# Kernel optimization log

Hardware: AMD Instinct MI355X
Metric: run time of the kernel (lower is better)

## Reference

```python
import jax, jax.numpy as jnp
import numpy as np

V = 131072          # total vertices (hits) across all events
K = 64              # neighbours per vertex, col 0 == self
NSEG = 4            # number of events (row splits segments)
THRESHOLD = 0.5     # hierarchy score cut (layer's non-trainable threshold var)


def setup_inputs() -> dict:
    key = jax.random.key(0)
    k1, k2 = jax.random.split(key)
    score = jax.random.uniform(k1, (V, 1), dtype=jnp.float32)
    seg = V // NSEG
    base = (jnp.arange(V, dtype=jnp.int32) // seg) * seg
    # random neighbours constrained to the same segment; column 0 is self
    rnd = jax.random.randint(k2, (V, K - 1), 0, seg, dtype=jnp.int32) + base[:, None]
    nidxs = jnp.concatenate([jnp.arange(V, dtype=jnp.int32)[:, None], rnd], axis=1)
    row_splits = (jnp.arange(NSEG + 1, dtype=jnp.int32) * seg)
    return {"score": score, "nidxs": nidxs, "row_splits": row_splits}


def _local_group(score1, nidxs, row_splits, thr):
    """Greedy threshold-based neighbour grouping (HGCalML LocalGroup op).

    Vertices are visited per segment in descending score order. An unused
    vertex becomes a group seed; if its score > thr it absorbs all of its
    not-yet-used neighbours. Returns fixed-shape (-1 padded) outputs so the
    whole thing is jit-compatible.
    """
    V_, K_ = nidxs.shape
    seg_id = jnp.searchsorted(row_splits, jnp.arange(V_, dtype=row_splits.dtype),
                              side='right') - 1
    # per-segment descending-score order == tf.argsort(DESC) per row split
    order = jnp.lexsort((-score1, seg_id)).astype(jnp.int32)
    kcols = jnp.arange(K_)

    def step(state, v):
        used, assign, dirn, sel, seed, count = state
        is_new = jnp.logical_not(used[v])                 # v not grouped yet -> seed
        expand = score1[v] > thr                          # absorb neighbours?
        cand = jnp.where(expand, nidxs[v],
                         jnp.where(kcols == 0, v, -1))    # else only self
        safe = jnp.clip(cand, 0, V_ - 1)
        valid = (cand >= 0) & jnp.logical_not(used[safe]) & is_new
        used = used.at[safe].set(used[safe] | valid)
        assign = assign.at[safe].set(jnp.where(valid, count, assign[safe]))
        dirn = dirn.at[v].set(jnp.where(valid, cand, -1))
        sel = sel.at[count].set(jnp.where(is_new, v, sel[count]))
        seed = seed.at[v].set(seed[v] | is_new)
        count = count + is_new.astype(jnp.int32)
        return (used, assign, dirn, sel, seed, count), None

    init = (jnp.zeros(V_, dtype=bool),                 # used
            jnp.full(V_, -1, jnp.int32),               # backgather: seed rank per vertex
            jnp.full((V_, K_), -1, jnp.int32),         # directed neighbour idxs
            jnp.full(V_, -1, jnp.int32),               # selected seed vertices, -1 padded
            jnp.zeros(V_, dtype=bool),                 # seed mask
            jnp.int32(0))
    (used, assign, dirn, sel, seed, count), _ = jax.lax.scan(step, init, order)
    cs0 = jnp.concatenate([jnp.zeros(1, jnp.int32),
                           jnp.cumsum(seed.astype(jnp.int32))])
    rs_new = cs0[row_splits]                           # new row splits over seeds
    return rs_new, dirn, sel[:, None], assign, count


def reference(score, nidxs, row_splits):
    # layer: score = clip(score, 0, 1); per-segment argsort; LocalGroup
    score1 = jnp.clip(score.reshape(-1), 0.0, 1.0)
    rs_new, dirnidx, sel, backgather, n_sel = _local_group(score1, nidxs,
                                                           row_splits, THRESHOLD)
    # return_backscatter=True -> back = [V, sel]; we return sel (padded) + n_sel
    # outputs: directed nidx (V,K), selection idxs (V,1 padded with -1),
    #          backgather (V,), new row splits, number selected
    return dirnidx, sel, backgather, rs_new, n_sel
```

## Files before the change

kernel.cpp:

```cpp
#include <hip/hip_runtime.h>
#include <stdint.h>

#define INFU 0xFFFFFFFFu
#define LCAP 32768
#define POSCAP 20480
#define NC 128

__global__ void __launch_bounds__(256) k_hist(const float* score, unsigned* bcnt,
                                              unsigned* claim, int* sel, unsigned* segE,
                                              int V, int SEGN, int initClaim){
  int v = blockIdx.x*blockDim.x+threadIdx.x; if (v>=V) return;
  if (initClaim) claim[v]=INFU;
  sel[v]=-1;
  float s = score[v]; s = fminf(fmaxf(s,0.f),1.f);
  int seg = v / SEGN;
  bool ex = (s > 0.5f);
  unsigned long long act = __ballot(true);
  unsigned long long mex = __ballot(ex);
  int lane = threadIdx.x & 63;
  int seg0 = __shfl(seg, 0);
  bool uni = (act == ~0ull) && (__shfl(seg,63) == seg0);
  if (uni){
    if (lane==0 && mex) atomicAdd(&segE[seg0], (unsigned)__popcll(mex));
  } else {
    if (ex) atomicAdd(&segE[seg], 1u);
  }
  int b = (int)(s*(float)SEGN); if (b>=SEGN) b=SEGN-1; if (b<0) b=0;
  int bd = SEGN-1-b;
  atomicAdd(&bcnt[(size_t)seg*SEGN+bd], 1u);
}

__global__ void __launch_bounds__(1024) k_scan0(const unsigned* bcnt, unsigned* bbase,
                                                unsigned* bfill, int SEGN){
  int seg = blockIdx.x; int tid = threadIdx.x; int lane = tid&63, wv = tid>>6;
  __shared__ unsigned s_wc[1024];
  const size_t base = (size_t)seg*SEGN;
  const int NP = (SEGN+1023)>>10;
  for (int p=0;p<NP;p++){
    int i = p*1024 + tid;
    unsigned x = (i<SEGN)? bcnt[base+i] : 0u;
    unsigned incl = x;
    #pragma unroll
    for (int off=1;off<64;off<<=1){ unsigned t=__shfl_up(incl,(unsigned)off); if (lane>=off) incl+=t; }
    if (lane==63) s_wc[p*16+wv]=incl;
  }
  __syncthreads();
  if (wv==0){
    unsigned carry=0; int n=NP*16;
    for (int ch=0; ch*64<n; ch++){
      int idx=ch*64+lane;
      unsigned x=(idx<n)? s_wc[idx]:0u;
      unsigned incl=x;
      #pragma unroll
      for (int off=1;off<64;off<<=1){ unsigned t=__shfl_up(incl,(unsigned)off); if (lane>=off) incl+=t; }
      if (idx<n) s_wc[idx]=carry+incl-x;
      carry += __shfl(incl,63);
    }
  }
  __syncthreads();
  for (int p=0;p<NP;p++){
    int i = p*1024 + tid;
    if (i<SEGN){
      unsigned x = bcnt[base+i];
      unsigned incl = x;
      #pragma unroll
      for (int off=1;off<64;off<<=1){ unsigned t=__shfl_up(incl,(unsigned)off); if (lane>=off) incl+=t; }
      bbase[base+i] = s_wc[p*16+wv] + incl - x;
      bfill[base+i] = 0u;
    }
  }
}

__global__ void __launch_bounds__(1024) k_scan(const unsigned* in, const unsigned* claim,
                                               unsigned* outExcl, unsigned* segTotal,
                                               int SEGN, int mode){
  int seg = blockIdx.x; int tid = threadIdx.x; int lane = tid&63, wv = tid>>6;
  __shared__ unsigned wsum[16];
  const int CH = (SEGN+1023)>>10;
  int i0 = tid*CH, i1 = i0+CH; if (i1>SEGN) i1=SEGN;
  const size_t base = (size_t)seg*SEGN;
  unsigned sum=0;
  for (int i=i0;i<i1;i++){
    unsigned x = (mode==0)? in[base+i] : ((claim[base+i]==INFU)?1u:0u);
    sum+=x;
  }
  unsigned incl=sum;
  for (int off=1;off<64;off<<=1){ unsigned t=__shfl_up(incl,(unsigned)off); if (lane>=off) incl+=t; }
  if (lane==63) wsum[wv]=incl;
  __syncthreads();
  unsigned wbase=0,total=0;
  for (int w=0;w<16;w++){ unsigned s=wsum[w]; if (w<wv) wbase+=s; total+=s; }
  unsigned run = wbase + incl - sum;
  for (int i=i0;i<i1;i++){
    unsigned x = (mode==0)? in[base+i] : ((claim[base+i]==INFU)?1u:0u);
    outExcl[base+i]=run; run+=x;
  }
  if (tid==0 && segTotal) segTotal[seg]=total;
}

__global__ void __launch_bounds__(256) k_scatter(const float* score, const unsigned* bbase,
                                                 unsigned* bfill, unsigned long long* slot,
                                                 int V, int SEGN){
  int v = blockIdx.x*blockDim.x+threadIdx.x; if (v>=V) return;
  float s = score[v]; s=fminf(fmaxf(s,0.f),1.f);
  int b=(int)(s*(float)SEGN); if(b>=SEGN)b=SEGN-1; if(b<0)b=0;
  int bd=SEGN-1-b; int seg=v/SEGN;
  size_t bk = (size_t)seg*SEGN+bd;
  unsigned pos = bbase[bk] + atomicAdd(&bfill[bk],1u);
  unsigned kb = ~__float_as_uint(s);
  slot[(size_t)seg*SEGN+pos] = ((unsigned long long)kb<<32) | (unsigned)v;
}

__global__ void __launch_bounds__(256) k_bsortbuild(const unsigned* bcnt, const unsigned* bbase,
                                                    unsigned long long* slot,
                                                    int* ord, unsigned* rnkv,
                                                    int V, int SEGN){
  int t = blockIdx.x*blockDim.x+threadIdx.x; if (t>=V) return;
  unsigned n = bcnt[t];
  if (!n) return;
  int seg = t / SEGN;
  const size_t segbase = (size_t)seg*SEGN;
  unsigned base = bbase[t];
  unsigned long long* a = slot + segbase + base;
  for (unsigned i=1;i<n;i++){
    unsigned long long key=a[i]; int j=(int)i-1;
    while (j>=0 && a[j]>key){ a[j+1]=a[j]; j--; }
    a[j+1]=key;
  }
  for (unsigned i=0;i<n;i++){
    int v = (int)(unsigned)(a[i] & 0xFFFFFFFFull);
    ord[segbase + base + i] = v;
    rnkv[v] = base + i;
  }
}

__global__ void __launch_bounds__(256) k_pack4(const int* ord, const unsigned* rnkv, const int* nidxs,
                                               const unsigned* segE, unsigned short* nbr16,
                                               int V, int K, int SEGN){
  const int K4 = K>>2;
  long long q = (long long)blockIdx.x*256 + threadIdx.x;
  if (q >= (long long)V*K4) return;
  int gr = (int)(q / K4); int k4 = (int)(q - (long long)gr*K4);
  int seg = gr / SEGN, r = gr - seg*SEGN;
  if (r >= (int)segE[seg]) return;
  int v = ord[gr];
  const int4 nn = *(const int4*)(nidxs + (size_t)v*K + (size_t)k4*4);
  ushort4 o;
  o.x=(unsigned short)rnkv[nn.x]; o.y=(unsigned short)rnkv[nn.y];
  o.z=(unsigned short)rnkv[nn.z]; o.w=(unsigned short)rnkv[nn.w];
  *(ushort4*)(nbr16 + (size_t)gr*K + (size_t)k4*4) = o;
}
__global__ void __launch_bounds__(256) k_pack(const int* ord, const unsigned* rnkv, const int* nidxs,
                                              const unsigned* segE, unsigned short* nbr16,
                                              int V, int K, int SEGN){
  long long t = (long long)blockIdx.x*256 + threadIdx.x;
  if (t >= (long long)V*K) return;
  int gr = (int)(t / K); int k = (int)(t - (long long)gr*K);
  int seg = gr / SEGN, r = gr - seg*SEGN;
  if (r >= (int)segE[seg]) return;
  int v = ord[gr];
  int w = nidxs[(size_t)v*K + k];
  nbr16[t] = (unsigned short)rnkv[w];
}

__global__ void __launch_bounds__(1024) k_greedy(const unsigned short* nbr16, const int* nidxs,
                                                 const int* ord, const unsigned* rnkv,
                                                 const unsigned* segEp,
                                                 unsigned* claim, unsigned* srank,
                                                 unsigned* segTotal, unsigned* absorb,
                                                 int SEGN, int K){
  __shared__ unsigned s_cl[LCAP/2];
  __shared__ unsigned short s_rnk[LCAP];
  __shared__ unsigned char s_pos[POSCAP];
  __shared__ unsigned s_cand[NC];
  __shared__ unsigned long long s_McLo[NC];
  __shared__ unsigned long long s_McHi[NC];
  __shared__ unsigned long long s_anyLo, s_anyHi;
  __shared__ unsigned long long s_bm[16];
  __shared__ unsigned s_ws[16];
  __shared__ unsigned s_base;
  __shared__ unsigned s_wcur;
  __shared__ unsigned long long s_v0, s_v1;
  const int seg = blockIdx.x, tid = threadIdx.x, lane = tid&63, wv = tid>>6;
  unsigned* clg = claim + (size_t)seg*SEGN;
  const size_t segbase = (size_t)seg*SEGN;
  const int E = (int)segEp[seg];
  const int cap = (LCAP < SEGN) ? LCAP : SEGN;
  const bool useDirect = (cap == SEGN);
  const int capw = (cap+1)>>1;
  for (int i=tid; i<capw; i+=1024) s_cl[i]=0xFFFFFFFFu;
  for (int i=tid; i<((POSCAP+3)>>2); i+=1024) ((unsigned*)s_pos)[i]=0u;
  if (useDirect){
    for (int i=tid; i<SEGN; i+=1024) s_rnk[i] = (unsigned short)rnkv[segbase + i];
  }
  if (tid<NC) s_cand[tid]=INFU;
  const unsigned long long lt_mask = (lane==0) ? 0ull : ((~0ull) >> (64-lane));
  const int li = (lane<K)? lane : 0;
  unsigned wcursor = 0;
  for (;;){
    __syncthreads();
    if (tid<NC){
      unsigned pc = s_cand[tid];
      if (pc!=INFU && pc<(unsigned)POSCAP) s_pos[pc]=0;
      s_cand[tid]=INFU; s_McLo[tid]=0ull; s_McHi[tid]=0ull;
    }
    if (tid==NC)   s_anyLo=0ull;
    if (tid==NC+1) s_anyHi=0ull;
    int found = 0;
    for (;;){
      unsigned r = wcursor + (unsigned)(wv*64 + lane);
      bool undec=false;
      if (r<(unsigned)E){
        if (r<(unsigned)cap)
          undec = (((s_cl[r>>1]>>((r&1)*16))&0xFFFFu)==0xFFFFu);
        else
          undec = (__hip_atomic_load(&clg[r], __ATOMIC_RELAXED, __HIP_MEMORY_SCOPE_AGENT)==INFU);
      }
      unsigned long long m = __ballot(undec);
      if (lane==0) s_bm[wv]=m;
      __syncthreads();
      unsigned long long mb = (lane<16)? s_bm[lane] : 0ull;
      int pc16 = (int)__popcll(mb);
      int incl = pc16;
      #pragma unroll
      for (int off=1; off<16; off<<=1){ int t=__shfl_up(incl,off); if (lane>=off) incl+=t; }
      int total = __shfl(incl, 15);
      int below = __shfl(incl, wv) - __shfl(pc16, wv);
      int pos = found + below + (int)__popcll(m & lt_mask);
      if (undec && pos<NC){
        s_cand[pos]=r;
        if (r<(unsigned)POSCAP) s_pos[r]=(unsigned char)(pos+1);
      }
      if (undec && pos==NC-1) s_wcur=r+1;
      bool filled = (found+total>=NC);
      bool winend = (wcursor + 1024 >= (unsigned)E);
      __syncthreads();
      if (filled){ wcursor = s_wcur; found=NC; break; }
      found += total;
      if (winend){ wcursor=(unsigned)E; break; }
      wcursor += 1024;
    }
    const int ncand = found;
    if (!ncand) break;
    unsigned rwq[8], cq[8];
    #pragma unroll
    for (int q=0;q<8;q++){
      int c=(wv<<3)|q;
      cq[q] = (c<ncand) ? s_cand[c] : INFU;
    }
    if (useDirect){
      int vq[8], nq[8];
      #pragma unroll
      for (int q=0;q<8;q++){
        unsigned cc = (cq[q]!=INFU)? cq[q] : 0u;
        vq[q] = ord[segbase + cc];
      }
      #pragma unroll
      for (int q=0;q<8;q++)
        nq[q] = nidxs[(size_t)vq[q]*K + li];
      #pragma unroll
      for (int q=0;q<8;q++){
        unsigned lv = (unsigned)(nq[q] - (int)segbase);
        unsigned rr = s_rnk[lv];
        rwq[q] = (cq[q]!=INFU && lane<K) ? rr : INFU;
      }
    } else {
      #pragma unroll
      for (int q=0;q<8;q++){
        rwq[q]=INFU;
        if (cq[q]!=INFU && lane<K)
          rwq[q] = (unsigned)nbr16[(segbase + cq[q])*K + lane];
      }
    }
    const bool fastmap = (s_cand[ncand-1] < (unsigned)POSCAP);
    #pragma unroll
    for (int q=0;q<8;q++){
      int c=(wv<<3)|q;
      if (cq[q]!=INFU){
        unsigned rw = rwq[q];
        int p = -1;
        if (fastmap){
          if (rw<(unsigned)POSCAP){ p = (int)s_pos[rw] - 1; }
        } else {
          int pp=0;
          if (s_cand[pp+64]<=rw) pp+=64;
          if (s_cand[pp+32]<=rw) pp+=32;
          if (s_cand[pp+16]<=rw) pp+=16;
          if (s_cand[pp+8 ]<=rw) pp+=8;
          if (s_cand[pp+4 ]<=rw) pp+=4;
          if (s_cand[pp+2 ]<=rw) pp+=2;
          if (s_cand[pp+1 ]<=rw) pp+=1;
          if (pp<ncand && s_cand[pp]==rw) p=pp;
        }
        if (lane<K && p>c){
          if (p<64){ atomicOr(&s_McLo[c], 1ull<<p);      atomicOr(&s_anyLo, 1ull<<p); }
          else     { atomicOr(&s_McHi[c], 1ull<<(p-64)); atomicOr(&s_anyHi, 1ull<<(p-64)); }
        }
      }
    }
    __syncthreads();
    if (wv==0){
      const int n0 = (ncand<64)? ncand : 64;
      const int n1 = ncand - n0;
      const unsigned long long nmask0 = (n0==64)? ~0ull : ((1ull<<n0)-1ull);
      unsigned long long Mj0 = s_McLo[lane];
      unsigned long long any0 = s_anyLo & nmask0;
      unsigned long long valid0 = (~any0) & nmask0;
      unsigned long long rem = any0;
      while (rem){
        int i=__builtin_ctzll(rem); rem &= rem-1;
        bool pred = ((valid0>>lane)&1ull) && (lane<i) && ((Mj0>>i)&1ull);
        if (__ballot(pred)==0ull) valid0 |= (1ull<<i);
      }
      unsigned long long valid1 = 0ull;
      if (n1>0){
        const unsigned long long nmask1 = (n1==64)? ~0ull : ((1ull<<n1)-1ull);
        unsigned long long sp = ((valid0>>lane)&1ull) ? s_McHi[lane] : 0ull;
        #pragma unroll
        for (int off=32; off; off>>=1)
          sp |= (unsigned long long)__shfl_xor((long long)sp, off);
        unsigned long long Mj1 = s_McHi[64+lane];
        unsigned long long any1 = s_anyHi & nmask1;
        valid1 = (~(any1|sp)) & nmask1;
        unsigned long long rem1 = any1 & ~sp;
        while (rem1){
          int i=__builtin_ctzll(rem1); rem1 &= rem1-1;
          bool pred = ((valid1>>lane)&1ull) && (lane<i) && ((Mj1>>i)&1ull);
          if (__ballot(pred)==0ull) valid1 |= (1ull<<i);
        }
      }
      if (lane==0){ s_v0=valid0; s_v1=valid1; }
    }
    __syncthreads();
    const unsigned long long v0 = s_v0, v1 = s_v1;
    #pragma unroll
    for (int q=0;q<8;q++){
      int c=(wv<<3)|q;
      bool isv = (c<64) ? (((v0>>c)&1ull)!=0ull) : (((v1>>(c-64))&1ull)!=0ull);
      if (cq[q]!=INFU && isv){
        unsigned rw=rwq[q], cr=cq[q];
        if (rw>cr && rw!=INFU){
          if (rw<(unsigned)cap){
            unsigned idx=rw>>1, sh=(rw&1)*16;
            unsigned old=s_cl[idx];
            for(;;){
              unsigned curv=(old>>sh)&0xFFFFu;
              if (cr>=curv) break;
              unsigned neu=(old & ~(0xFFFFu<<sh)) | (cr<<sh);
              unsigned prev=atomicCAS(&s_cl[idx], old, neu);
              if (prev==old) break;
              old=prev;
            }
          } else {
            atomicMin(&clg[rw], cr);
          }
        }
      }
    }
  }
  __syncthreads();
  if (cap == SEGN){
    if (tid==0) s_base=0;
    __syncthreads();
    for (int p=0; p<cap; p+=1024){
      int i = p + tid;
      bool live = (i<cap);
      unsigned c16 = 0xFFFFu;
      if (live) c16 = (s_cl[i>>1]>>((i&1)*16))&0xFFFFu;
      bool isSeed = live && (c16==0xFFFFu);
      unsigned long long m = __ballot(isSeed);
      if (lane==0) s_ws[wv]=(unsigned)__popcll(m);
      __syncthreads();
      unsigned wbase=0, tot=0;
      for (int w2=0;w2<16;w2++){ unsigned t2=s_ws[w2]; if (w2<wv) wbase+=t2; tot+=t2; }
      unsigned ex = s_base + wbase + (unsigned)__popcll(m & lt_mask);
      if (live){
        srank[segbase + i] = ex;
        absorb[ord[segbase + i]] = isSeed ? (unsigned)i : (unsigned)c16;
      }
      __syncthreads();
      if (tid==0) s_base += tot;
    }
    __syncthreads();
    if (tid==0) segTotal[seg] = s_base;
  } else {
    for (int r=tid; r<cap; r+=1024){
      unsigned c=(s_cl[r>>1]>>((r&1)*16))&0xFFFFu;
      clg[r] = (c==0xFFFFu) ? INFU : c;
    }
  }
}

__global__ void __launch_bounds__(256) k_absorb(const unsigned* rnkv, const unsigned* claim,
                                                unsigned* absorb, int V, int SEGN){
  int v = blockIdx.x*blockDim.x+threadIdx.x; if (v>=V) return;
  int seg = v / SEGN;
  unsigned r = rnkv[v];
  unsigned c = claim[(size_t)seg*SEGN + r];
  absorb[v] = (c==INFU)? r : c;
}

__global__ void __launch_bounds__(256) k_dirnAll4(const int* nidxs, const unsigned* rnkv,
                                                  const unsigned* absorb, const float* score,
                                                  const unsigned* segTotal,
                                                  const unsigned* srank,
                                                  int* dirn, int* sel, int* backg,
                                                  int* rs, int* nsel,
                                                  int V, int K, int SEGN, int NSEG){
  const int K4 = K>>2;
  long long q = (long long)blockIdx.x*256 + threadIdx.x;
  if (q >= (long long)V*K4) return;
  int v = (int)(q / K4); int k4 = (int)(q - (long long)v*K4);
  int seg = v / SEGN;
  if (q <= (long long)NSEG){
    unsigned run=0;
    for (int s=0;s<(int)q;s++) run+=segTotal[s];
    rs[q]=(int)run;
    if ((int)q==NSEG) nsel[0]=(int)run;
  }
  unsigned r = rnkv[v];
  unsigned a_self = absorb[v];
  bool seed = (a_self == r);
  if (k4==0){
    unsigned segOff=0;
    for (int s=0;s<seg;s++) segOff+=segTotal[s];
    unsigned g = segOff + srank[(size_t)seg*SEGN + a_self];
    backg[v] = (int)g;
    if (seed) sel[g] = v;
  }
  int4 o = make_int4(-1,-1,-1,-1);
  if (seed){
    float s = score[v]; s=fminf(fmaxf(s,0.f),1.f);
    if (!(s > 0.5f)){
      if (k4==0) o.x = v;
    } else {
      const int4 nn = *(const int4*)(nidxs + (size_t)v*K + (size_t)k4*4);
      if (absorb[nn.x]==r) o.x=nn.x;
      if (absorb[nn.y]==r) o.y=nn.y;
      if (absorb[nn.z]==r) o.z=nn.z;
      if (absorb[nn.w]==r) o.w=nn.w;
    }
  }
  *(int4*)(dirn + (size_t)v*K + (size_t)k4*4) = o;
}
__global__ void __launch_bounds__(256) k_dirnAll(const int* nidxs, const unsigned* rnkv,
                                                 const unsigned* absorb, const float* score,
                                                 const unsigned* segTotal,
                                                 const unsigned* srank,
                                                 int* dirn, int* sel, int* backg,
                                                 int* rs, int* nsel,
                                                 int V, int K, int SEGN, int NSEG){
  long long t = (long long)blockIdx.x*blockDim.x + threadIdx.x;
  if (t >= (long long)V*K) return;
  int v = (int)(t / K); int j = (int)(t - (long long)v*K);
  int seg = v / SEGN;
  if (t <= (long long)NSEG){
    unsigned run=0;
    for (int s=0;s<(int)t;s++) run+=segTotal[s];
    rs[t]=(int)run;
    if ((int)t==NSEG) nsel[0]=(int)run;
  }
  unsigned r = rnkv[v];
  unsigned a_self = absorb[v];
  bool seed = (a_self == r);
  if (j==0){
    unsigned segOff=0;
    for (int s=0;s<seg;s++) segOff+=segTotal[s];
    unsigned g = segOff + srank[(size_t)seg*SEGN + a_self];
    backg[v] = (int)g;
    if (seed) sel[g] = v;
  }
  int out = -1;
  if (seed){
    float s = score[v]; s=fminf(fmaxf(s,0.f),1.f);
    if (!(s > 0.5f)){
      out = (j==0)? v : -1;
    } else {
      int w = nidxs[(size_t)v*K + j];
      out = (absorb[w] == r)? w : -1;
    }
  }
  dirn[t] = out;
}

extern "C" void kernel_launch(void* const* d_in, const int* in_sizes, int n_in,
                              void* d_out, int out_size, void* d_ws, size_t ws_size,
                              hipStream_t stream) {
  const float* score   = (const float*)d_in[0];
  const int*   nidxs   = (const int*)d_in[1];
  (void)d_in[2];

  const int V    = in_sizes[0];
  const int K    = in_sizes[1] / V;
  const int NSEG = in_sizes[2] - 1;
  const int SEGN = V / NSEG;

  char* w = (char*)d_ws;
  unsigned long long* slot = (unsigned long long*)w;  w += (size_t)V*8;
  unsigned* bcnt  = (unsigned*)w; w += (size_t)V*4;
  unsigned* segE  = (unsigned*)w; w += 64;
  unsigned* bfill = (unsigned*)w; w += (size_t)V*4;
  unsigned* bbase = (unsigned*)w; w += (size_t)V*4;
  int*      ord   = (int*)w;      w += (size_t)V*4;
  unsigned* rnkv  = (unsigned*)w; w += (size_t)V*4;
  unsigned* claim = (unsigned*)w; w += (size_t)V*4;
  unsigned* srank = (unsigned*)w; w += (size_t)V*4;
  unsigned* segTotal = (unsigned*)w; w += 64;
  unsigned* absorb = bcnt;

  int* out      = (int*)d_out;
  int* out_dirn = out;
  int* out_sel  = out + (size_t)V*K;
  int* out_bg   = out_sel + V;
  int* out_rs   = out_bg + V;
  int* out_nsel = out_rs + (NSEG+1);

  unsigned short* nbr16 = (unsigned short*)out_dirn;

  hipMemsetAsync(bcnt, 0x00, (size_t)V*4 + 64, stream);

  int nb256 = (V + 255)/256;
  long long totVK = (long long)V*K;
  int nbVK = (int)((totVK + 255)/256);
  const bool vec4 = (K>=4) && ((K&3)==0);
  int nbQ = (int)(((long long)V*(K>>2) + 255)/256);
  const int initClaim = (SEGN > LCAP) ? 1 : 0;

  k_hist<<<nb256, 256, 0, stream>>>(score, bcnt, claim, out_sel, segE, V, SEGN, initClaim);
  k_scan0<<<NSEG, 1024, 0, stream>>>(bcnt, bbase, bfill, SEGN);
  k_scatter<<<nb256, 256, 0, stream>>>(score, bbase, bfill, slot, V, SEGN);
  k_bsortbuild<<<nb256, 256, 0, stream>>>(bcnt, bbase, slot, ord, rnkv, V, SEGN);
  if (SEGN > LCAP){
    if (vec4) k_pack4<<<nbQ, 256, 0, stream>>>(ord, rnkv, nidxs, segE, nbr16, V, K, SEGN);
    else      k_pack <<<nbVK, 256, 0, stream>>>(ord, rnkv, nidxs, segE, nbr16, V, K, SEGN);
  }
  k_greedy<<<NSEG, 1024, 0, stream>>>(nbr16, nidxs, ord, rnkv, segE, claim, srank, segTotal,
                                      absorb, SEGN, K);
  if (SEGN > LCAP){
    k_scan<<<NSEG, 1024, 0, stream>>>(nullptr, claim, srank, segTotal, SEGN, 1);
    k_absorb<<<nb256, 256, 0, stream>>>(rnkv, claim, absorb, V, SEGN);
  }
  if (vec4) k_dirnAll4<<<nbQ, 256, 0, stream>>>(nidxs, rnkv, absorb, score, segTotal, srank,
                                                out_dirn, out_sel, out_bg, out_rs, out_nsel,
                                                V, K, SEGN, NSEG);
  else      k_dirnAll<<<nbVK, 256, 0, stream>>>(nidxs, rnkv, absorb, score, segTotal, srank,
                                                out_dirn, out_sel, out_bg, out_rs, out_nsel,
                                                V, K, SEGN, NSEG);
}
```

Measured before the change: 317.7 us.

## Fuse whole LocalGroup pipeline into one cooperative kernel with grid syncs

Replaces the chain of histogram, scan, scatter, bucket-sort, greedy, and output kernels with a single cooperative kernel of 256 blocks of 1024 threads that separates the phases with grid.sync. The aim is to remove per-launch overhead and the separate memset between the small phases. The greedy phase still runs on only NSEG blocks while the rest of the grid waits at the barrier. The non-fused fallback path is also simplified to always pack neighbour ranks into global memory, with the greedy merging its result into the global claim array via min. Risks are cooperative-launch limits with large LDS per block, and whether a grid sync costs less than a kernel launch.

```diff
diff --git a/kernel.cpp b/kernel.cpp
--- a/kernel.cpp
+++ b/kernel.cpp
@@ -1,10 +1,398 @@
 #include <hip/hip_runtime.h>
+#include <hip/hip_cooperative_groups.h>
 #include <stdint.h>
+
+namespace cg = cooperative_groups;
 
 #define INFU 0xFFFFFFFFu
 #define LCAP 32768
 #define POSCAP 20480
 #define NC 128
+
+__global__ void __launch_bounds__(1024) k_fused(const float* score, const int* nidxs,
+                                                unsigned* bcnt, unsigned* segE,
+                                                unsigned* bfill, unsigned* bbase,
+                                                unsigned long long* slot, int* ord,
+                                                unsigned* rnkv, unsigned* srank,
+                                                unsigned* segTotal, unsigned* absorb,
+                                                int* dirn, int* sel, int* backg,
+                                                int* rs, int* nsel,
+                                                int V, int K, int SEGN, int NSEG){
+  cg::grid_group grid = cg::this_grid();
+  __shared__ unsigned s_cl[LCAP/2];
+  __shared__ unsigned short s_rnk[LCAP];
+  __shared__ unsigned char s_pos[POSCAP];
+  __shared__ unsigned s_cand[NC];
+  __shared__ unsigned long long s_McLo[NC];
+  __shared__ unsigned long long s_McHi[NC];
+  __shared__ unsigned long long s_anyLo, s_anyHi;
+  __shared__ unsigned long long s_bm[16];
+  __shared__ unsigned s_ws[16];
+  __shared__ unsigned s_base;
+  __shared__ unsigned s_wcur;
+  __shared__ unsigned long long s_v0, s_v1;
+
+  const int tid = threadIdx.x, lane = tid&63, wv = tid>>6;
+  const long long gidx = (long long)blockIdx.x*1024 + tid;
+  const long long gstride = (long long)gridDim.x*1024;
+  const unsigned long long lt_mask = (lane==0) ? 0ull : ((~0ull) >> (64-lane));
+
+  for (long long i=gidx; i<V; i+=gstride) bcnt[i]=0u;
+  if (gidx < NSEG) segE[gidx]=0u;
+  grid.sync();
+
+  for (long long vv=gidx; vv<V; vv+=gstride){
+    int v = (int)vv;
+    sel[v]=-1;
+    float s = score[v]; s = fminf(fmaxf(s,0.f),1.f);
+    int seg = v / SEGN;
+    bool ex = (s > 0.5f);
+    unsigned long long act = __ballot(true);
+    unsigned long long mex = __ballot(ex);
+    int seg0 = __shfl(seg, 0);
+    bool uni = (act == ~0ull) && (__shfl(seg,63) == seg0);
+    if (uni){
+      if (lane==0 && mex) atomicAdd(&segE[seg0], (unsigned)__popcll(mex));
+    } else {
+      if (ex) atomicAdd(&segE[seg], 1u);
+    }
+    int b = (int)(s*(float)SEGN); if (b>=SEGN) b=SEGN-1; if (b<0) b=0;
+    int bd = SEGN-1-b;
+    atomicAdd(&bcnt[(size_t)seg*SEGN+bd], 1u);
+  }
+  grid.sync();
+
+  if (blockIdx.x < (unsigned)NSEG){
+    unsigned* s_wc = (unsigned*)s_pos;
+    int seg = blockIdx.x;
+    const size_t base = (size_t)seg*SEGN;
+    const int NP = (SEGN+1023)>>10;
+    for (int p=0;p<NP;p++){
+      int i = p*1024 + tid;
+      unsigned x = (i<SEGN)? bcnt[base+i] : 0u;
+      unsigned incl = x;
+      #pragma unroll
+      for (int off=1;off<64;off<<=1){ unsigned t=__shfl_up(incl,(unsigned)off); if (lane>=off) incl+=t; }
+      if (lane==63) s_wc[p*16+wv]=incl;
+    }
+    __syncthreads();
+    if (wv==0){
+      unsigned carry=0; int n=NP*16;
+      for (int ch=0; ch*64<n; ch++){
+        int idx=ch*64+lane;
+        unsigned x=(idx<n)? s_wc[idx]:0u;
+        unsigned incl=x;
+        #pragma unroll
+        for (int off=1;off<64;off<<=1){ unsigned t=__shfl_up(incl,(unsigned)off); if (lane>=off) incl+=t; }
+        if (idx<n) s_wc[idx]=carry+incl-x;
+        carry += __shfl(incl,63);
+      }
+    }
+    __syncthreads();
+    for (int p=0;p<NP;p++){
+      int i = p*1024 + tid;
+      if (i<SEGN){
+        unsigned x = bcnt[base+i];
+        unsigned incl = x;
+        #pragma unroll
+        for (int off=1;off<64;off<<=1){ unsigned t=__shfl_up(incl,(unsigned)off); if (lane>=off) incl+=t; }
+        bbase[base+i] = s_wc[p*16+wv] + incl - x;
+        bfill[base+i] = 0u;
+      }
+    }
+  }
+  grid.sync();
+
+  for (long long vv=gidx; vv<V; vv+=gstride){
+    int v = (int)vv;
+    float s = score[v]; s=fminf(fmaxf(s,0.f),1.f);
+    int b=(int)(s*(float)SEGN); if(b>=SEGN)b=SEGN-1; if(b<0)b=0;
+    int bd=SEGN-1-b; int seg=v/SEGN;
+    size_t bk = (size_t)seg*SEGN+bd;
+    unsigned pos = bbase[bk] + atomicAdd(&bfill[bk],1u);
+    unsigned kb = ~__float_as_uint(s);
+    slot[(size_t)seg*SEGN+pos] = ((unsigned long long)kb<<32) | (unsigned)v;
+  }
+  grid.sync();
+
+  for (long long tt=gidx; tt<V; tt+=gstride){
+    int t = (int)tt;
+    unsigned n = bcnt[t];
+    if (!n) continue;
+    int seg = t / SEGN;
+    const size_t segbase = (size_t)seg*SEGN;
+    unsigned base = bbase[t];
+    unsigned long long* a = slot + segbase + base;
+    for (unsigned i=1;i<n;i++){
+      unsigned long long key=a[i]; int j=(int)i-1;
+      while (j>=0 && a[j]>key){ a[j+1]=a[j]; j--; }
+      a[j+1]=key;
+    }
+    for (unsigned i=0;i<n;i++){
+      int v = (int)(unsigned)(a[i] & 0xFFFFFFFFull);
+      ord[segbase + base + i] = v;
+      rnkv[v] = base + i;
+    }
+  }
+  grid.sync();
+
+  if (blockIdx.x < (unsigned)NSEG){
+    const int seg = blockIdx.x;
+    const size_t segbase = (size_t)seg*SEGN;
+    const int E = (int)segE[seg];
+    const int capw = (SEGN+1)>>1;
+    for (int i=tid; i<capw; i+=1024) s_cl[i]=0xFFFFFFFFu;
+    for (int i=tid; i<((POSCAP+3)>>2); i+=1024) ((unsigned*)s_pos)[i]=0u;
+    for (int i=tid; i<SEGN; i+=1024) s_rnk[i] = (unsigned short)rnkv[segbase + i];
+    if (tid<NC) s_cand[tid]=INFU;
+    const int li = (lane<K)? lane : 0;
+    unsigned wcursor = 0;
+    for (;;){
+      __syncthreads();
+      if (tid<NC){
+        unsigned pc = s_cand[tid];
+        if (pc!=INFU && pc<(unsigned)POSCAP) s_pos[pc]=0;
+        s_cand[tid]=INFU; s_McLo[tid]=0ull; s_McHi[tid]=0ull;
+      }
+      if (tid==NC)   s_anyLo=0ull;
+      if (tid==NC+1) s_anyHi=0ull;
+      int found = 0;
+      for (;;){
+        unsigned r = wcursor + (unsigned)(wv*64 + lane);
+        bool undec=false;
+        if (r<(unsigned)E)
+          undec = (((s_cl[r>>1]>>((r&1)*16))&0xFFFFu)==0xFFFFu);
+        unsigned long long m = __ballot(undec);
+        if (lane==0) s_bm[wv]=m;
+        __syncthreads();
+        unsigned long long mb = (lane<16)? s_bm[lane] : 0ull;
+        int pc16 = (int)__popcll(mb);
+        int incl = pc16;
+        #pragma unroll
+        for (int off=1; off<16; off<<=1){ int t=__shfl_up(incl,off); if (lane>=off) incl+=t; }
+        int total = __shfl(incl, 15);
+        int below = __shfl(incl, wv) - __shfl(pc16, wv);
+        int pos = found + below + (int)__popcll(m & lt_mask);
+        if (undec && pos<NC){
+          s_cand[pos]=r;
+          if (r<(unsigned)POSCAP) s_pos[r]=(unsigned char)(pos+1);
+        }
+        if (undec && pos==NC-1) s_wcur=r+1;
+        bool filled = (found+total>=NC);
+        bool winend = (wcursor + 1024 >= (unsigned)E);
+        __syncthreads();
+        if (filled){ wcursor = s_wcur; found=NC; break; }
+        found += total;
+        if (winend){ wcursor=(unsigned)E; break; }
+        wcursor += 1024;
+      }
+      const int ncand = found;
+      if (!ncand) break;
+      unsigned rwq[8], cq[8];
+      #pragma unroll
+      for (int q=0;q<8;q++){
+        int c=(wv<<3)|q;
+        cq[q] = (c<ncand) ? s_cand[c] : INFU;
+      }
+      {
+        int vq[8], nq[8];
+        #pragma unroll
+        for (int q=0;q<8;q++){
+          unsigned cc = (cq[q]!=INFU)? cq[q] : 0u;
+          vq[q] = ord[segbase + cc];
+        }
+        #pragma unroll
+        for (int q=0;q<8;q++)
+          nq[q] = nidxs[(size_t)vq[q]*K + li];
+        #pragma unroll
+        for (int q=0;q<8;q++){
+          unsigned lv = (unsigned)(nq[q] - (int)segbase);
+          unsigned rr = s_rnk[lv];
+          rwq[q] = (cq[q]!=INFU && lane<K) ? rr : INFU;
+        }
+      }
+      const bool fastmap = (s_cand[ncand-1] < (unsigned)POSCAP);
+      #pragma unroll
+      for (int q=0;q<8;q++){
+        int c=(wv<<3)|q;
+        if (cq[q]!=INFU){
+          unsigned rw = rwq[q];
+          int p = -1;
+          if (fastmap){
+            if (rw<(unsigned)POSCAP){ p = (int)s_pos[rw] - 1; }
+          } else {
+            int pp=0;
+            if (s_cand[pp+64]<=rw) pp+=64;
+            if (s_cand[pp+32]<=rw) pp+=32;
+            if (s_cand[pp+16]<=rw) pp+=16;
+            if (s_cand[pp+8 ]<=rw) pp+=8;
+            if (s_cand[pp+4 ]<=rw) pp+=4;
+            if (s_cand[pp+2 ]<=rw) pp+=2;
+            if (s_cand[pp+1 ]<=rw) pp+=1;
+            if (pp<ncand && s_cand[pp]==rw) p=pp;
+          }
+          if (lane<K && p>c){
+            if (p<64){ atomicOr(&s_McLo[c], 1ull<<p);      atomicOr(&s_anyLo, 1ull<<p); }
+            else     { atomicOr(&s_McHi[c], 1ull<<(p-64)); atomicOr(&s_anyHi, 1ull<<(p-64)); }
+          }
+        }
+      }
+      __syncthreads();
+      if (wv==0){
+        const int n0 = (ncand<64)? ncand : 64;
+        const int n1 = ncand - n0;
+        const unsigned long long nmask0 = (n0==64)? ~0ull : ((1ull<<n0)-1ull);
+        unsigned long long Mj0 = s_McLo[lane];
+        unsigned long long any0 = s_anyLo & nmask0;
+        unsigned long long valid0 = (~any0) & nmask0;
+        unsigned long long rem = any0;
+        while (rem){
+          int i=__builtin_ctzll(rem); rem &= rem-1;
+          bool pred = ((valid0>>lane)&1ull) && (lane<i) && ((Mj0>>i)&1ull);
+          if (__ballot(pred)==0ull) valid0 |= (1ull<<i);
+        }
+        unsigned long long valid1 = 0ull;
+        if (n1>0){
+          const unsigned long long nmask1 = (n1==64)? ~0ull : ((1ull<<n1)-1ull);
+          unsigned long long sp = ((valid0>>lane)&1ull) ? s_McHi[lane] : 0ull;
+          #pragma unroll
+          for (int off=32; off; off>>=1)
+            sp |= (unsigned long long)__shfl_xor((long long)sp, off);
+          unsigned long long Mj1 = s_McHi[64+lane];
+          unsigned long long any1 = s_anyHi & nmask1;
+          valid1 = (~(any1|sp)) & nmask1;
+          unsigned long long rem1 = any1 & ~sp;
+          while (rem1){
+            int i=__builtin_ctzll(rem1); rem1 &= rem1-1;
+            bool pred = ((valid1>>lane)&1ull) && (lane<i) && ((Mj1>>i)&1ull);
+            if (__ballot(pred)==0ull) valid1 |= (1ull<<i);
+          }
+        }
+        if (lane==0){ s_v0=valid0; s_v1=valid1; }
+      }
+      __syncthreads();
+      const unsigned long long v0 = s_v0, v1 = s_v1;
+      #pragma unroll
+      for (int q=0;q<8;q++){
+        int c=(wv<<3)|q;
+        bool isv = (c<64) ? (((v0>>c)&1ull)!=0ull) : (((v1>>(c-64))&1ull)!=0ull);
+        if (cq[q]!=INFU && isv){
+          unsigned rw=rwq[q], cr=cq[q];
+          if (rw>cr && rw!=INFU){
+            unsigned idx=rw>>1, sh=(rw&1)*16;
+            unsigned old=s_cl[idx];
+            for(;;){
+              unsigned curv=(old>>sh)&0xFFFFu;
+              if (cr>=curv) break;
+              unsigned neu=(old & ~(0xFFFFu<<sh)) | (cr<<sh);
+              unsigned prev=atomicCAS(&s_cl[idx], old, neu);
+              if (prev==old) break;
+              old=prev;
+            }
+          }
+        }
+      }
+    }
+    __syncthreads();
+    if (tid==0) s_base=0;
+    __syncthreads();
+    for (int p=0; p<SEGN; p+=1024){
+      int i = p + tid;
+      bool live = (i<SEGN);
+      unsigned c16 = 0xFFFFu;
+      if (live) c16 = (s_cl[i>>1]>>((i&1)*16))&0xFFFFu;
+      bool isSeed = live && (c16==0xFFFFu);
+      unsigned long long m = __ballot(isSeed);
+      if (lane==0) s_ws[wv]=(unsigned)__popcll(m);
+      __syncthreads();
+      unsigned wbase=0, tot=0;
+      for (int w2=0;w2<16;w2++){ unsigned t2=s_ws[w2]; if (w2<wv) wbase+=t2; tot+=t2; }
+      unsigned ex = s_base + wbase + (unsigned)__popcll(m & lt_mask);
+      if (live){
+        srank[segbase + i] = ex;
+        absorb[ord[segbase + i]] = isSeed ? (unsigned)i : (unsigned)c16;
+      }
+      __syncthreads();
+      if (tid==0) s_base += tot;
+    }
+    __syncthreads();
+    if (tid==0) segTotal[seg] = s_base;
+    __threadfence();
+  }
+  grid.sync();
+
+  if (K>=4 && (K&3)==0){
+    const int K4 = K>>2;
+    const long long tot = (long long)V*K4;
+    for (long long q=gidx; q<tot; q+=gstride){
+      int v = (int)(q / K4); int k4 = (int)(q - (long long)v*K4);
+      int seg = v / SEGN;
+      if (q <= (long long)NSEG){
+        unsigned run=0;
+        for (int s=0;s<(int)q;s++) run+=segTotal[s];
+        rs[q]=(int)run;
+        if ((int)q==NSEG) nsel[0]=(int)run;
+      }
+      unsigned r = rnkv[v];
+      unsigned a_self = absorb[v];
+      bool seed = (a_self == r);
+      if (k4==0){
+        unsigned segOff=0;
+        for (int s=0;s<seg;s++) segOff+=segTotal[s];
+        unsigned g = segOff + srank[(size_t)seg*SEGN + a_self];
+        backg[v] = (int)g;
+        if (seed) sel[g] = v;
+      }
+      int4 o = make_int4(-1,-1,-1,-1);
+      if (seed){
+        float s = score[v]; s=fminf(fmaxf(s,0.f),1.f);
+        if (!(s > 0.5f)){
+          if (k4==0) o.x = v;
+        } else {
+          const int4 nn = *(const int4*)(nidxs + (size_t)v*K + (size_t)k4*4);
+          if (absorb[nn.x]==r) o.x=nn.x;
+          if (absorb[nn.y]==r) o.y=nn.y;
+          if (absorb[nn.z]==r) o.z=nn.z;
+          if (absorb[nn.w]==r) o.w=nn.w;
+        }
+      }
+      *(int4*)(dirn + (size_t)v*K + (size_t)k4*4) = o;
+    }
+  } else {
+    const long long tot = (long long)V*K;
+    for (long long t=gidx; t<tot; t+=gstride){
+      int v = (int)(t / K); int j = (int)(t - (long long)v*K);
+      int seg = v / SEGN;
+      if (t <= (long long)NSEG){
+        unsigned run=0;
+        for (int s=0;s<(int)t;s++) run+=segTotal[s];
+        rs[t]=(int)run;
+        if ((int)t==NSEG) nsel[0]=(int)run;
+      }
+      unsigned r = rnkv[v];
+      unsigned a_self = absorb[v];
+      bool seed = (a_self == r);
+      if (j==0){
+        unsigned segOff=0;
+        for (int s=0;s<seg;s++) segOff+=segTotal[s];
+        unsigned g = segOff + srank[(size_t)seg*SEGN + a_self];
+        backg[v] = (int)g;
+        if (seed) sel[g] = v;
+      }
+      int out = -1;
+      if (seed){
+        float s = score[v]; s=fminf(fmaxf(s,0.f),1.f);
+        if (!(s > 0.5f)){
+          out = (j==0)? v : -1;
+        } else {
+          int w = nidxs[(size_t)v*K + j];
+          out = (absorb[w] == r)? w : -1;
+        }
+      }
+      dirn[t] = out;
+    }
+  }
+}
 
 __global__ void __launch_bounds__(256) k_hist(const float* score, unsigned* bcnt,
                                               unsigned* claim, int* sel, unsigned* segE,
@@ -163,22 +551,16 @@
   nbr16[t] = (unsigned short)rnkv[w];
 }
 
-__global__ void __launch_bounds__(1024) k_greedy(const unsigned short* nbr16, const int* nidxs,
-                                                 const int* ord, const unsigned* rnkv,
+__global__ void __launch_bounds__(1024) k_greedy(const unsigned short* nbr16,
                                                  const unsigned* segEp,
-                                                 unsigned* claim, unsigned* srank,
-                                                 unsigned* segTotal, unsigned* absorb,
-                                                 int SEGN, int K){
+                                                 unsigned* claim, int SEGN, int K){
   __shared__ unsigned s_cl[LCAP/2];
-  __shared__ unsigned short s_rnk[LCAP];
   __shared__ unsigned char s_pos[POSCAP];
   __shared__ unsigned s_cand[NC];
   __shared__ unsigned long long s_McLo[NC];
   __shared__ unsigned long long s_McHi[NC];
   __shared__ unsigned long long s_anyLo, s_anyHi;
   __shared__ unsigned long long s_bm[16];
-  __shared__ unsigned s_ws[16];
-  __shared__ unsigned s_base;
   __shared__ unsigned s_wcur;
   __shared__ unsigned long long s_v0, s_v1;
   const int seg = blockIdx.x, tid = threadIdx.x, lane = tid&63, wv = tid>>6;
@@ -186,16 +568,11 @@
   const size_t segbase = (size_t)seg*SEGN;
   const int E = (int)segEp[seg];
   const int cap = (LCAP < SEGN) ? LCAP : SEGN;
-  const bool useDirect = (cap == SEGN);
   const int capw = (cap+1)>>1;
   for (int i=tid; i<capw; i+=1024) s_cl[i]=0xFFFFFFFFu;
   for (int i=tid; i<((POSCAP+3)>>2); i+=1024) ((unsigned*)s_pos)[i]=0u;
-  if (useDirect){
-    for (int i=tid; i<SEGN; i+=1024) s_rnk[i] = (unsigned short)rnkv[segbase + i];
-  }
   if (tid<NC) s_cand[tid]=INFU;
   const unsigned long long lt_mask = (lane==0) ? 0ull : ((~0ull) >> (64-lane));
-  const int li = (lane<K)? lane : 0;
   unsigned wcursor = 0;
   for (;;){
     __syncthreads();
@@ -248,29 +625,11 @@
       int c=(wv<<3)|q;
       cq[q] = (c<ncand) ? s_cand[c] : INFU;
     }
-    if (useDirect){
-      int vq[8], nq[8];
-      #pragma unroll
-      for (int q=0;q<8;q++){
-        unsigned cc = (cq[q]!=INFU)? cq[q] : 0u;
-        vq[q] = ord[segbase + cc];
-      }
-      #pragma unroll
-      for (int q=0;q<8;q++)
-        nq[q] = nidxs[(size_t)vq[q]*K + li];
-      #pragma unroll
-      for (int q=0;q<8;q++){
-        unsigned lv = (unsigned)(nq[q] - (int)segbase);
-        unsigned rr = s_rnk[lv];
-        rwq[q] = (cq[q]!=INFU && lane<K) ? rr : INFU;
-      }
-    } else {
-      #pragma unroll
-      for (int q=0;q<8;q++){
-        rwq[q]=INFU;
-        if (cq[q]!=INFU && lane<K)
-          rwq[q] = (unsigned)nbr16[(segbase + cq[q])*K + lane];
-      }
+    #pragma unroll
+    for (int q=0;q<8;q++){
+      rwq[q]=INFU;
+      if (cq[q]!=INFU && lane<K)
+        rwq[q] = (unsigned)nbr16[(segbase + cq[q])*K + lane];
     }
     const bool fastmap = (s_cand[ncand-1] < (unsigned)POSCAP);
     #pragma unroll
@@ -359,35 +718,11 @@
     }
   }
   __syncthreads();
-  if (cap == SEGN){
-    if (tid==0) s_base=0;
-    __syncthreads();
-    for (int p=0; p<cap; p+=1024){
-      int i = p + tid;
-      bool live = (i<cap);
-      unsigned c16 = 0xFFFFu;
-      if (live) c16 = (s_cl[i>>1]>>((i&1)*16))&0xFFFFu;
-      bool isSeed = live && (c16==0xFFFFu);
-      unsigned long long m = __ballot(isSeed);
-      if (lane==0) s_ws[wv]=(unsigned)__popcll(m);
-      __syncthreads();
-      unsigned wbase=0, tot=0;
-      for (int w2=0;w2<16;w2++){ unsigned t2=s_ws[w2]; if (w2<wv) wbase+=t2; tot+=t2; }
-      unsigned ex = s_base + wbase + (unsigned)__popcll(m & lt_mask);
-      if (live){
-        srank[segbase + i] = ex;
-        absorb[ord[segbase + i]] = isSeed ? (unsigned)i : (unsigned)c16;
-      }
-      __syncthreads();
-      if (tid==0) s_base += tot;
-    }
-    __syncthreads();
-    if (tid==0) segTotal[seg] = s_base;
-  } else {
-    for (int r=tid; r<cap; r+=1024){
-      unsigned c=(s_cl[r>>1]>>((r&1)*16))&0xFFFFu;
-      clg[r] = (c==0xFFFFu) ? INFU : c;
-    }
+  for (int r=tid; r<cap; r+=1024){
+    unsigned c=(s_cl[r>>1]>>((r&1)*16))&0xFFFFu;
+    unsigned g = clg[r];
+    unsigned m = (c<g)? c : g;
+    clg[r] = m;
   }
 }
 
@@ -517,6 +852,23 @@
 
   unsigned short* nbr16 = (unsigned short*)out_dirn;
 
+  const bool useFused = (SEGN <= LCAP) && (NSEG <= 256) && (K <= 64);
+
+  if (useFused){
+    void* args[] = {
+      (void*)&score, (void*)&nidxs,
+      (void*)&bcnt, (void*)&segE, (void*)&bfill, (void*)&bbase,
+      (void*)&slot, (void*)&ord, (void*)&rnkv, (void*)&srank,
+      (void*)&segTotal, (void*)&absorb,
+      (void*)&out_dirn, (void*)&out_sel, (void*)&out_bg,
+      (void*)&out_rs, (void*)&out_nsel,
+      (void*)&V, (void*)&K, (void*)&SEGN, (void*)&NSEG
+    };
+    hipLaunchCooperativeKernel((const void*)k_fused, dim3(256), dim3(1024),
+                               args, 0, stream);
+    return;
+  }
+
   hipMemsetAsync(bcnt, 0x00, (size_t)V*4 + 64, stream);
 
   int nb256 = (V + 255)/256;
@@ -524,22 +876,16 @@
   int nbVK = (int)((totVK + 255)/256);
   const bool vec4 = (K>=4) && ((K&3)==0);
   int nbQ = (int)(((long long)V*(K>>2) + 255)/256);
-  const int initClaim = (SEGN > LCAP) ? 1 : 0;
-
-  k_hist<<<nb256, 256, 0, stream>>>(score, bcnt, claim, out_sel, segE, V, SEGN, initClaim);
+
+  k_hist<<<nb256, 256, 0, stream>>>(score, bcnt, claim, out_sel, segE, V, SEGN, 1);
   k_scan0<<<NSEG, 1024, 0, stream>>>(bcnt, bbase, bfill, SEGN);
   k_scatter<<<nb256, 256, 0, stream>>>(score, bbase, bfill, slot, V, SEGN);
   k_bsortbuild<<<nb256, 256, 0, stream>>>(bcnt, bbase, slot, ord, rnkv, V, SEGN);
-  if (SEGN > LCAP){
-    if (vec4) k_pack4<<<nbQ, 256, 0, stream>>>(ord, rnkv, nidxs, segE, nbr16, V, K, SEGN);
-    else      k_pack <<<nbVK, 256, 0, stream>>>(ord, rnkv, nidxs, segE, nbr16, V, K, SEGN);
-  }
-  k_greedy<<<NSEG, 1024, 0, stream>>>(nbr16, nidxs, ord, rnkv, segE, claim, srank, segTotal,
-                                      absorb, SEGN, K);
-  if (SEGN > LCAP){
-    k_scan<<<NSEG, 1024, 0, stream>>>(nullptr, claim, srank, segTotal, SEGN, 1);
-    k_absorb<<<nb256, 256, 0, stream>>>(rnkv, claim, absorb, V, SEGN);
-  }
+  if (vec4) k_pack4<<<nbQ, 256, 0, stream>>>(ord, rnkv, nidxs, segE, nbr16, V, K, SEGN);
+  else      k_pack <<<nbVK, 256, 0, stream>>>(ord, rnkv, nidxs, segE, nbr16, V, K, SEGN);
+  k_greedy<<<NSEG, 1024, 0, stream>>>(nbr16, segE, claim, SEGN, K);
+  k_scan<<<NSEG, 1024, 0, stream>>>(nullptr, claim, srank, segTotal, SEGN, 1);
+  k_absorb<<<nb256, 256, 0, stream>>>(rnkv, claim, absorb, V, SEGN);
   if (vec4) k_dirnAll4<<<nbQ, 256, 0, stream>>>(nidxs, rnkv, absorb, score, segTotal, srank,
                                                 out_dirn, out_sel, out_bg, out_rs, out_nsel,
                                                 V, K, SEGN, NSEG);
```

Measured after the change: 459.0 us. +44.5%, slower.

## Prefill dirn with memset and launch per-vertex final kernel writing only seed rows

Applied to the files above, without the earlier changes.

Replaces the per-(vertex,k4) dirn kernel with a per-vertex kernel that writes backgather/sel and, for seeds only, loops over the neighbour row. It writes only the surviving entries. The -1 fill of dirn moves to a hipMemsetAsync issued before the pipeline on the fast path, or after the slow-path scan when nbr16 aliases dirn. Non-seed vertices no longer read nidxs or gather absorb. The trade-off is that each seed thread runs a long serial loop with uncoalesced row accesses, which lowers parallelism.

```diff
diff --git a/kernel.cpp b/kernel.cpp
--- a/kernel.cpp
+++ b/kernel.cpp
@@ -400,87 +400,49 @@
   absorb[v] = (c==INFU)? r : c;
 }
 
-__global__ void __launch_bounds__(256) k_dirnAll4(const int* nidxs, const unsigned* rnkv,
-                                                  const unsigned* absorb, const float* score,
-                                                  const unsigned* segTotal,
-                                                  const unsigned* srank,
-                                                  int* dirn, int* sel, int* backg,
-                                                  int* rs, int* nsel,
-                                                  int V, int K, int SEGN, int NSEG){
-  const int K4 = K>>2;
-  long long q = (long long)blockIdx.x*256 + threadIdx.x;
-  if (q >= (long long)V*K4) return;
-  int v = (int)(q / K4); int k4 = (int)(q - (long long)v*K4);
+__global__ void __launch_bounds__(256) k_final(const int* nidxs, const unsigned* rnkv,
+                                               const unsigned* absorb, const float* score,
+                                               const unsigned* segTotal, const unsigned* srank,
+                                               int* dirn, int* sel, int* backg,
+                                               int* rs, int* nsel,
+                                               int V, int K, int SEGN, int NSEG){
+  int v = blockIdx.x*256 + threadIdx.x;
+  if (v >= V) return;
   int seg = v / SEGN;
-  if (q <= (long long)NSEG){
+  if (v <= NSEG){
     unsigned run=0;
-    for (int s=0;s<(int)q;s++) run+=segTotal[s];
-    rs[q]=(int)run;
-    if ((int)q==NSEG) nsel[0]=(int)run;
+    for (int s=0;s<v;s++) run+=segTotal[s];
+    rs[v]=(int)run;
+    if (v==NSEG) nsel[0]=(int)run;
   }
   unsigned r = rnkv[v];
   unsigned a_self = absorb[v];
   bool seed = (a_self == r);
-  if (k4==0){
-    unsigned segOff=0;
-    for (int s=0;s<seg;s++) segOff+=segTotal[s];
-    unsigned g = segOff + srank[(size_t)seg*SEGN + a_self];
-    backg[v] = (int)g;
-    if (seed) sel[g] = v;
-  }
-  int4 o = make_int4(-1,-1,-1,-1);
-  if (seed){
-    float s = score[v]; s=fminf(fmaxf(s,0.f),1.f);
-    if (!(s > 0.5f)){
-      if (k4==0) o.x = v;
-    } else {
+  unsigned segOff=0;
+  for (int s=0;s<seg;s++) segOff+=segTotal[s];
+  unsigned g = segOff + srank[(size_t)seg*SEGN + a_self];
+  backg[v] = (int)g;
+  if (!seed) return;
+  sel[g] = v;
+  float s = score[v]; s=fminf(fmaxf(s,0.f),1.f);
+  int* drow = dirn + (size_t)v*K;
+  if (!(s > 0.5f)){
+    drow[0] = v;
+  } else if ((K&3)==0){
+    const int K4 = K>>2;
+    for (int k4=0;k4<K4;k4++){
       const int4 nn = *(const int4*)(nidxs + (size_t)v*K + (size_t)k4*4);
-      if (absorb[nn.x]==r) o.x=nn.x;
-      if (absorb[nn.y]==r) o.y=nn.y;
-      if (absorb[nn.z]==r) o.z=nn.z;
-      if (absorb[nn.w]==r) o.w=nn.w;
-    }
-  }
-  *(int4*)(dirn + (size_t)v*K + (size_t)k4*4) = o;
-}
-__global__ void __launch_bounds__(256) k_dirnAll(const int* nidxs, const unsigned* rnkv,
-                                                 const unsigned* absorb, const float* score,
-                                                 const unsigned* segTotal,
-                                                 const unsigned* srank,
-                                                 int* dirn, int* sel, int* backg,
-                                                 int* rs, int* nsel,
-                                                 int V, int K, int SEGN, int NSEG){
-  long long t = (long long)blockIdx.x*blockDim.x + threadIdx.x;
-  if (t >= (long long)V*K) return;
-  int v = (int)(t / K); int j = (int)(t - (long long)v*K);
-  int seg = v / SEGN;
-  if (t <= (long long)NSEG){
-    unsigned run=0;
-    for (int s=0;s<(int)t;s++) run+=segTotal[s];
-    rs[t]=(int)run;
-    if ((int)t==NSEG) nsel[0]=(int)run;
-  }
-  unsigned r = rnkv[v];
-  unsigned a_self = absorb[v];
-  bool seed = (a_self == r);
-  if (j==0){
-    unsigned segOff=0;
-    for (int s=0;s<seg;s++) segOff+=segTotal[s];
-    unsigned g = segOff + srank[(size_t)seg*SEGN + a_self];
-    backg[v] = (int)g;
-    if (seed) sel[g] = v;
-  }
-  int out = -1;
-  if (seed){
-    float s = score[v]; s=fminf(fmaxf(s,0.f),1.f);
-    if (!(s > 0.5f)){
-      out = (j==0)? v : -1;
-    } else {
-      int w = nidxs[(size_t)v*K + j];
-      out = (absorb[w] == r)? w : -1;
-    }
-  }
-  dirn[t] = out;
+      if (absorb[nn.x]==r) drow[k4*4+0]=nn.x;
+      if (absorb[nn.y]==r) drow[k4*4+1]=nn.y;
+      if (absorb[nn.z]==r) drow[k4*4+2]=nn.z;
+      if (absorb[nn.w]==r) drow[k4*4+3]=nn.w;
+    }
+  } else {
+    for (int j=0;j<K;j++){
+      int w2 = nidxs[(size_t)v*K + j];
+      if (absorb[w2]==r) drow[j]=w2;
+    }
+  }
 }
 
 extern "C" void kernel_launch(void* const* d_in, const int* in_sizes, int n_in,
@@ -517,33 +479,34 @@
 
   unsigned short* nbr16 = (unsigned short*)out_dirn;
 
-  hipMemsetAsync(bcnt, 0x00, (size_t)V*4 + 64, stream);
-
   int nb256 = (V + 255)/256;
   long long totVK = (long long)V*K;
   int nbVK = (int)((totVK + 255)/256);
   const bool vec4 = (K>=4) && ((K&3)==0);
   int nbQ = (int)(((long long)V*(K>>2) + 255)/256);
   const int initClaim = (SEGN > LCAP) ? 1 : 0;
+  const bool fastPath = (SEGN <= LCAP);
+
+  if (fastPath)
+    hipMemsetAsync(out_dirn, 0xFF, (size_t)V*K*4, stream);
+  hipMemsetAsync(bcnt, 0x00, (size_t)V*4 + 64, stream);
 
   k_hist<<<nb256, 256, 0, stream>>>(score, bcnt, claim, out_sel, segE, V, SEGN, initClaim);
   k_scan0<<<NSEG, 1024, 0, stream>>>(bcnt, bbase, bfill, SEGN);
   k_scatter<<<nb256, 256, 0, stream>>>(score, bbase, bfill, slot, V, SEGN);
   k_bsortbuild<<<nb256, 256, 0, stream>>>(bcnt, bbase, slot, ord, rnkv, V, SEGN);
-  if (SEGN > LCAP){
+  if (!fastPath){
     if (vec4) k_pack4<<<nbQ, 256, 0, stream>>>(ord, rnkv, nidxs, segE, nbr16, V, K, SEGN);
     else      k_pack <<<nbVK, 256, 0, stream>>>(ord, rnkv, nidxs, segE, nbr16, V, K, SEGN);
   }
   k_greedy<<<NSEG, 1024, 0, stream>>>(nbr16, nidxs, ord, rnkv, segE, claim, srank, segTotal,
                                       absorb, SEGN, K);
-  if (SEGN > LCAP){
+  if (!fastPath){
     k_scan<<<NSEG, 1024, 0, stream>>>(nullptr, claim, srank, segTotal, SEGN, 1);
     k_absorb<<<nb256, 256, 0, stream>>>(rnkv, claim, absorb, V, SEGN);
-  }
-  if (vec4) k_dirnAll4<<<nbQ, 256, 0, stream>>>(nidxs, rnkv, absorb, score, segTotal, srank,
-                                                out_dirn, out_sel, out_bg, out_rs, out_nsel,
-                                                V, K, SEGN, NSEG);
-  else      k_dirnAll<<<nbVK, 256, 0, stream>>>(nidxs, rnkv, absorb, score, segTotal, srank,
-                                                out_dirn, out_sel, out_bg, out_rs, out_nsel,
-                                                V, K, SEGN, NSEG);
-}
+    hipMemsetAsync(out_dirn, 0xFF, (size_t)V*K*4, stream);
+  }
+  k_final<<<nb256, 256, 0, stream>>>(nidxs, rnkv, absorb, score, segTotal, srank,
+                                     out_dirn, out_sel, out_bg, out_rs, out_nsel,
+                                     V, K, SEGN, NSEG);
+}
```

Result: slower. 330.3 us (+4.0%).
